# Kernel tuning notes

Hardware: AMD Instinct MI355X
Metric: run time of the kernel (lower is better)

The kernel has to match this reference:

```python
import jax, jax.numpy as jnp
import numpy as np

S, B, E, H = 2048, 4, 512, 8
HD = E // H


def setup_inputs() -> dict:
    key = jax.random.key(0)
    ks = jax.random.split(key, 5)
    scale = 1.0 / np.sqrt(E)
    return {
        "query": jax.random.normal(ks[0], (S, B, E), jnp.float32),
        "key": jax.random.normal(ks[1], (S, B, E), jnp.float32),
        "value": jax.random.normal(ks[2], (S, B, E), jnp.float32),
        "in_proj_weight": jax.random.normal(ks[3], (3 * E, E), jnp.float32) * scale,
        "in_proj_bias": jnp.zeros((3 * E,), jnp.float32),
        "out_proj_weight": jax.random.normal(ks[4], (E, E), jnp.float32) * scale,
        "out_proj_bias": jnp.zeros((E,), jnp.float32),
    }


def reference(query, key, value, in_proj_weight, in_proj_bias, out_proj_weight, out_proj_bias):
    tgt_len, bsz, embed_dim = query.shape
    src_len = key.shape[0]
    # Quirk of this module: first chunk (w_qk) projects BOTH q and k; third chunk projects v.
    w_qk = in_proj_weight[:embed_dim]
    w_v = in_proj_weight[2 * embed_dim:]
    b_qk = in_proj_bias[:embed_dim]
    b_v = in_proj_bias[2 * embed_dim:]
    q = query @ w_qk.T + b_qk          # [S, B, E]
    k = key @ w_qk.T + b_qk
    v = value @ w_v.T + b_v
    # (S, B, E) -> (B*H, S, HD)
    def split_heads(x, n):
        return x.reshape(n, bsz * H, HD).transpose(1, 0, 2)
    q = split_heads(q, tgt_len) / jnp.sqrt(jnp.asarray(HD, q.dtype))
    k = split_heads(k, src_len)
    v = split_heads(v, src_len)
    scores = jnp.einsum("bqd,bkd->bqk", q, k)          # [B*H, S, S] full score matrix
    attn = jax.nn.softmax(scores, axis=-1)
    out = jnp.einsum("bqk,bkd->bqd", attn, v)          # [B*H, S, HD]
    out = out.transpose(1, 0, 2).reshape(tgt_len * bsz, embed_dim)
    out = out @ out_proj_weight.T + out_proj_bias
    return out.reshape(tgt_len, bsz, embed_dim)
```

## Files before the change

### kernel.cpp

```cpp
#include <hip/hip_runtime.h>
#include <hip/hip_bf16.h>

typedef __attribute__((ext_vector_type(8))) short s16x8;
typedef __attribute__((ext_vector_type(4))) short s16x4;
typedef __attribute__((ext_vector_type(4))) float f32x4;

#if __has_builtin(__builtin_amdgcn_exp2f)
#define EXP2F(x) __builtin_amdgcn_exp2f(x)
#else
#define EXP2F(x) exp2f(x)
#endif

#define S_LEN 2048
#define EMB   512
#define MROWS 8192

__device__ __forceinline__ short f2bf(float f) {
    union { float f; unsigned u; } z; z.f = f;
    unsigned r = z.u + 0x7FFF + ((z.u >> 16) & 1);
    return (short)(r >> 16);
}
__device__ __forceinline__ short f2bf_fast(float f) {
    union { float f; unsigned u; } z; z.f = f;
    return (short)((z.u + 0x8000u) >> 16);
}
__device__ __forceinline__ int swzs(int s) { return s ^ ((s >> 3) & 7); }

__device__ __forceinline__ void barrier_fast() {
    asm volatile("s_waitcnt lgkmcnt(0)" ::: "memory");
    __builtin_amdgcn_s_barrier();
    __builtin_amdgcn_sched_barrier(0);
}

__global__ __launch_bounds__(256) void w_to_bf16(const float* __restrict__ W,
                                                 short* __restrict__ wb, int n)
{
    int i = (blockIdx.x * 256 + threadIdx.x) * 8;
    if (i < n) {
        f32x4 a = *(const f32x4*)(W + i);
        f32x4 b = *(const f32x4*)(W + i + 4);
        s16x8 o;
        o[0] = f2bf(a[0]); o[1] = f2bf(a[1]); o[2] = f2bf(a[2]); o[3] = f2bf(a[3]);
        o[4] = f2bf(b[0]); o[5] = f2bf(b[1]); o[6] = f2bf(b[2]); o[7] = f2bf(b[3]);
        *(s16x8*)(wb + i) = o;
    }
}

template<int AF32, int BF32>
__device__ __forceinline__ void gemm_mainloop(const void* __restrict__ Ag,
                                              const void* __restrict__ Bg,
                                              short* sA, short* sB,
                                              f32x4 acc[2][4], int K)
{
    const int tid  = threadIdx.x;
    const int lane = tid & 63;
    const int wv   = tid >> 6;
    const int lsw  = lane ^ ((lane >> 3) & 7);
    const int amt  = (wv >> 1) * 2;
    const int bnt  = (wv & 1) * 4;

    const int brow = tid >> 2, bqd = tid & 3;
    const int boff = swzs((brow >> 4) * 64 + bqd * 16 + (brow & 15)) * 8;
    const int frow = tid >> 3, ffc = tid & 7;
    const int foff = swzs((frow >> 4) * 64 + (ffc >> 1) * 16 + (frow & 15)) * 8
                   + (ffc & 1) * 4;

    f32x4 aF0[2], aF1[2], bF0[2], bF1[2];
    s16x8 aH0, aH1, bH0, bH1;

    auto loadA = [&](int kt, f32x4 fr[2], s16x8& hr) {
        if (AF32) {
            const float* g = (const float*)Ag + (size_t)frow * K + kt + ffc * 4;
            fr[0] = *(const f32x4*)g;
            fr[1] = *(const f32x4*)(g + (size_t)64 * K);
        } else {
            hr = *(const s16x8*)((const short*)Ag + (size_t)brow * K + kt + bqd * 8);
        }
    };
    auto loadB = [&](int kt, f32x4 fr[2], s16x8& hr) {
        if (BF32) {
            const float* g = (const float*)Bg + (size_t)frow * K + kt + ffc * 4;
            fr[0] = *(const f32x4*)g;
            fr[1] = *(const f32x4*)(g + (size_t)64 * K);
        } else {
            hr = *(const s16x8*)((const short*)Bg + (size_t)brow * K + kt + bqd * 8);
        }
    };
    auto commit = [&](short* s, f32x4 fr[2], s16x8& hr, int F32) {
        if (F32) {
#pragma unroll
            for (int p = 0; p < 2; ++p) {
                s16x4 o4;
                o4[0] = f2bf_fast(fr[p][0]); o4[1] = f2bf_fast(fr[p][1]);
                o4[2] = f2bf_fast(fr[p][2]); o4[3] = f2bf_fast(fr[p][3]);
                *(s16x4*)(s + foff + p * 2048) = o4;
            }
        } else {
            *(s16x8*)(s + boff) = hr;
        }
    };
    auto compute = [&](const short* sAc, const short* sBc) {
        s16x8 a[2], b[4];
#pragma unroll
        for (int i = 0; i < 2; ++i)
            a[i] = *(const s16x8*)(sAc + ((amt + i) * 64 + lsw) * 8);
#pragma unroll
        for (int j = 0; j < 4; ++j)
            b[j] = *(const s16x8*)(sBc + ((bnt + j) * 64 + lsw) * 8);
#pragma unroll
        for (int i = 0; i < 2; ++i)
#pragma unroll
            for (int j = 0; j < 4; ++j)
                acc[i][j] = __builtin_amdgcn_mfma_f32_16x16x32_bf16(a[i], b[j], acc[i][j], 0, 0, 0);
    };

    loadA(0, aF0, aH0);  loadB(0, bF0, bH0);
    loadA(32, aF1, aH1); loadB(32, bF1, bH1);
    commit(sA, aF0, aH0, AF32); commit(sB, bF0, bH0, BF32);
    barrier_fast();

    for (int kt = 0; kt < K; kt += 64) {
        const int k2 = (kt + 64 < K) ? kt + 64 : 0;
        loadA(k2, aF0, aH0); loadB(k2, bF0, bH0);
        compute(sA, sB);
        commit(sA + 4096, aF1, aH1, AF32); commit(sB + 4096, bF1, bH1, BF32);
        barrier_fast();
        const int k3 = (kt + 96 < K) ? kt + 96 : 0;
        loadA(k3, aF1, aH1); loadB(k3, bF1, bH1);
        compute(sA + 4096, sB + 4096);
        commit(sA, aF0, aH0, AF32); commit(sB, bF0, bH0, BF32);
        barrier_fast();
    }
}

__global__ __launch_bounds__(512, 4) void qkv_proj(const float* __restrict__ query,
                                                   const float* __restrict__ key,
                                                   const float* __restrict__ value,
                                                   const short* __restrict__ wb,
                                                   const float* __restrict__ bias,
                                                   short* __restrict__ q,
                                                   short* __restrict__ k,
                                                   short* __restrict__ vt)
{
    __shared__ __align__(16) short smem[16384];
    short* sA = smem;
    short* sB = smem + 8192;

    const int z = blockIdx.z;
    const float* X  = (z == 0) ? query : (z == 1) ? key : value;
    const short* Wz = wb   + (z == 2 ? (size_t)1024 * EMB : 0);
    const float* bz = bias + (z == 2 ? 1024 : 0);
    const float scale = (z == 0) ? 0.125f * 1.44269504f : 1.0f;

    const int blockM = blockIdx.x * 128, blockN = blockIdx.y * 128;

    f32x4 acc[2][4];
#pragma unroll
    for (int i = 0; i < 2; ++i)
#pragma unroll
        for (int j = 0; j < 4; ++j)
            acc[i][j] = (f32x4){0.f, 0.f, 0.f, 0.f};

    gemm_mainloop<1, 0>(X + (size_t)blockM * EMB, Wz + (size_t)blockN * EMB,
                        sA, sB, acc, EMB);

    const int tid = threadIdx.x, lane = tid & 63, wv = tid >> 6;
    const int l15 = lane & 15, quad = lane >> 4;
    const int wm = (wv >> 1) * 32, wn = (wv & 1) * 64;

#pragma unroll
    for (int j = 0; j < 4; ++j) {
        int colL = wn + j * 16 + l15;
        float bval = bz[blockN + colL];
        int hL = colL >> 6, hd = colL & 63;
#pragma unroll
        for (int i = 0; i < 2; ++i) {
#pragma unroll
            for (int r = 0; r < 4; ++r) {
                int rowL = wm + i * 16 + quad * 4 + r;
                int b = rowL & 3, sp = rowL >> 2;
                float val = (acc[i][j][r] + bval) * scale;
                int idx;
                if (z == 2) {
                    int R = (b * 2 + hL) * 64 + hd;
                    idx = R * 32 + (((sp >> 3) ^ (R & 3)) << 3) + (sp & 7);
                } else {
                    idx = ((b * 2 + hL) * 32 + sp) * 64 + hd;
                }
                smem[idx] = f2bf(val);
            }
        }
    }
    barrier_fast();

    if (z == 2) {
        int R = tid;
        int b = tid >> 7, hL = (tid >> 6) & 1, hd = tid & 63;
        int h = (blockN >> 6) + hL;
        short* dst = vt + ((size_t)(b * 8 + h) * 64 + hd) * 2048 + (blockM >> 2);
#pragma unroll
        for (int u = 0; u < 4; ++u)
            ((s16x8*)dst)[u] = *(const s16x8*)(smem + R * 32 + ((u ^ (R & 3)) << 3));
    } else {
        const s16x8* src = (const s16x8*)(smem + tid * 32);
        int b = tid >> 7, hL = (tid >> 6) & 1;
        int sp = (tid >> 1) & 31, hdh = (tid & 1) * 32;
        int h = (blockN >> 6) + hL;
        short* dstp = (z == 0) ? q : k;
        short* dst = dstp + ((size_t)(b * 8 + h) * 2048 + (blockM >> 2) + sp) * 64 + hdh;
#pragma unroll
        for (int u = 0; u < 4; ++u) ((s16x8*)dst)[u] = src[u];
    }
}

__global__ __launch_bounds__(256, 2) void flash_attn(const short* __restrict__ q,
                                                     const short* __restrict__ k,
                                                     const short* __restrict__ vt,
                                                     short* __restrict__ attn)
{
    __shared__ __align__(16) short sK[2][8192];
    __shared__ __align__(16) short sV[2][8192];
    const int bh = blockIdx.x;
    const int q0 = blockIdx.y * 128;
    const int tid = threadIdx.x, wv = tid >> 6, lane = tid & 63;
    const int l15 = lane & 15, quad = lane >> 4;
    const int lsw = lane ^ ((lane >> 3) & 7);

    s16x8 qf[2][2];
#pragma unroll
    for (int qr = 0; qr < 2; ++qr) {
        const short* qp = q + ((size_t)(bh * 2048 + q0 + wv * 32 + qr * 16 + l15)) * 64 + quad * 8;
        qf[qr][0] = *(const s16x8*)qp;
        qf[qr][1] = *(const s16x8*)(qp + 32);
    }

    const short* kg = k  + (size_t)bh * 2048 * 64;
    const short* vg = vt + (size_t)bh * 64 * 2048;

    const int rk = tid >> 2, qd = tid & 3;
    const int pr = (rk & 35) | ((rk & 24) >> 1) | ((rk & 4) << 2);
    const int kw0 = swzs((pr >> 4) * 64 + qd * 16 + (pr & 15)) * 8;
    const int vw0 = swzs((rk >> 4) * 64 + qd * 16 + (rk & 15)) * 8;
    const short* kgt = kg + (size_t)rk * 64 + qd * 8;
    const short* vgt = vg + (size_t)rk * 2048 + qd * 8;

    f32x4 o[2][4];
    float ls[2][4];
#pragma unroll
    for (int qr = 0; qr < 2; ++qr)
#pragma unroll
        for (int i = 0; i < 4; ++i) { o[qr][i] = (f32x4){0.f, 0.f, 0.f, 0.f}; ls[qr][i] = 0.f; }

    s16x8 kr[2][2], vr[2][2];
    auto loadT = [&](int kt) {
#pragma unroll
        for (int s = 0; s < 2; ++s) {
            kr[s][0] = *(const s16x8*)(kgt + (size_t)(kt + s * 64) * 64);
            kr[s][1] = *(const s16x8*)(kgt + (size_t)(kt + s * 64) * 64 + 32);
            vr[s][0] = *(const s16x8*)(vgt + kt + s * 64);
            vr[s][1] = *(const s16x8*)(vgt + kt + s * 64 + 32);
        }
    };
    auto commitT = [&](int buf) {
#pragma unroll
        for (int s = 0; s < 2; ++s) {
            *(s16x8*)(sK[buf] + s * 4096 + kw0)        = kr[s][0];
            *(s16x8*)(sK[buf] + s * 4096 + kw0 + 2048) = kr[s][1];
            *(s16x8*)(sV[buf] + s * 4096 + vw0)        = vr[s][0];
            *(s16x8*)(sV[buf] + s * 4096 + vw0 + 2048) = vr[s][1];
        }
    };
    auto computeQK = [&](const short* Kc, f32x4 sc[2][4]) {
#pragma unroll
        for (int ct = 0; ct < 4; ++ct) {
            s16x8 kf0 = *(const s16x8*)(Kc + (ct * 64 + lsw) * 8);
            s16x8 kf1 = *(const s16x8*)(Kc + (ct * 64 + lsw) * 8 + 2048);
#pragma unroll
            for (int qr = 0; qr < 2; ++qr) {
                f32x4 c = (f32x4){0.f, 0.f, 0.f, 0.f};
                c = __builtin_amdgcn_mfma_f32_16x16x32_bf16(kf0, qf[qr][0], c, 0, 0, 0);
                c = __builtin_amdgcn_mfma_f32_16x16x32_bf16(kf1, qf[qr][1], c, 0, 0, 0);
                sc[qr][ct] = c;
            }
        }
    };
    auto softmaxPV = [&](f32x4 sc[2][4], const short* Vc) {
        s16x8 pf[2][2];
#pragma unroll
        for (int qr = 0; qr < 2; ++qr)
#pragma unroll
            for (int c = 0; c < 2; ++c)
#pragma unroll
                for (int h = 0; h < 2; ++h)
#pragma unroll
                    for (int r = 0; r < 4; ++r) {
                        float p = EXP2F(sc[qr][2 * c + h][r]);
                        ls[qr][r] += p;
                        pf[qr][c][h * 4 + r] = f2bf_fast(p);
                    }
#pragma unroll
        for (int nt = 0; nt < 4; ++nt)
#pragma unroll
            for (int c = 0; c < 2; ++c) {
                s16x8 vf = *(const s16x8*)(Vc + ((c * 4 + nt) * 64 + lsw) * 8);
#pragma unroll
                for (int qr = 0; qr < 2; ++qr)
                    o[qr][nt] = __builtin_amdgcn_mfma_f32_16x16x32_bf16(pf[qr][c], vf, o[qr][nt], 0, 0, 0);
            }
    };

    loadT(0);
    commitT(0);
    __syncthreads();

    int cur = 0;
    for (int kt = 0; kt < 2048; kt += 128) {
        loadT((kt + 128) & 2047);

        f32x4 sc0[2][4], sc1[2][4];
        computeQK(sK[cur], sc0);
        computeQK(sK[cur] + 4096, sc1);
        softmaxPV(sc0, sV[cur]);
        softmaxPV(sc1, sV[cur] + 4096);

        commitT(cur ^ 1);
        __syncthreads();
        cur ^= 1;
    }

    const int b = bh >> 3, h = bh & 7;
#pragma unroll
    for (int qr = 0; qr < 2; ++qr) {
        float s = ls[qr][0] + ls[qr][1] + ls[qr][2] + ls[qr][3];
        s += __shfl_xor(s, 16, 64);
        s += __shfl_xor(s, 32, 64);
        float sinv = 1.0f / s;
        float inv[4];
#pragma unroll
        for (int r = 0; r < 4; ++r)
            inv[r] = __shfl(sinv, quad * 20 + r, 64);
#pragma unroll
        for (int r = 0; r < 4; ++r) {
            int srow = q0 + wv * 32 + qr * 16 + quad * 4 + r;
#pragma unroll
            for (int nt = 0; nt < 4; ++nt)
                attn[(size_t)(srow * 4 + b) * 512 + h * 64 + nt * 16 + l15] = f2bf(o[qr][nt][r] * inv[r]);
        }
    }
}

__global__ __launch_bounds__(512, 4) void out_proj(const short* __restrict__ attn,
                                                   const float* __restrict__ W,
                                                   const float* __restrict__ bias,
                                                   float* __restrict__ out)
{
    __shared__ __align__(16) short sA[2 * 4096], sB[2 * 4096];
    const int blockM = blockIdx.x * 128, blockN = blockIdx.y * 128;

    f32x4 acc[2][4];
#pragma unroll
    for (int i = 0; i < 2; ++i)
#pragma unroll
        for (int j = 0; j < 4; ++j)
            acc[i][j] = (f32x4){0.f, 0.f, 0.f, 0.f};

    gemm_mainloop<0, 1>(attn + (size_t)blockM * EMB, W + (size_t)blockN * EMB,
                        sA, sB, acc, EMB);

    const int tid = threadIdx.x, lane = tid & 63, wv = tid >> 6;
    const int l15 = lane & 15, quad = lane >> 4;
    const int wm = (wv >> 1) * 32, wn = (wv & 1) * 64;

#pragma unroll
    for (int j = 0; j < 4; ++j) {
        int col = blockN + wn + j * 16 + l15;
        float bval = bias[col];
#pragma unroll
        for (int i = 0; i < 2; ++i) {
#pragma unroll
            for (int r = 0; r < 4; ++r) {
                int row = blockM + wm + i * 16 + quad * 4 + r;
                out[(size_t)row * 512 + col] = acc[i][j][r] + bval;
            }
        }
    }
}

extern "C" void kernel_launch(void* const* d_in, const int* in_sizes, int n_in,
                              void* d_out, int out_size, void* d_ws, size_t ws_size,
                              hipStream_t stream)
{
    const float* query = (const float*)d_in[0];
    const float* key   = (const float*)d_in[1];
    const float* value = (const float*)d_in[2];
    const float* ipw   = (const float*)d_in[3];
    const float* ipb   = (const float*)d_in[4];
    const float* opw   = (const float*)d_in[5];
    const float* opb   = (const float*)d_in[6];
    float* out = (float*)d_out;

    const size_t NELEM = (size_t)MROWS * EMB;
    short* q    = (short*)d_ws;
    short* k    = q + NELEM;
    short* attn = k + NELEM;
    short* vt   = (short*)d_out;
    short* wb   = (short*)d_out + NELEM;

    w_to_bf16 <<<dim3(384),      256, 0, stream>>>(ipw, wb, 1536 * EMB);
    qkv_proj  <<<dim3(64, 4, 3), 512, 0, stream>>>(query, key, value, wb, ipb, q, k, vt);
    flash_attn<<<dim3(32, 16),   256, 0, stream>>>(q, k, vt, attn);
    out_proj  <<<dim3(64, 4),    512, 0, stream>>>(attn, opw, opb, out);
}
```

Baseline: 181.3 us.

## Fuse all stages into one cooperative persistent kernel with grid syncs

Replaces the four separate launches (weight conversion, QKV projection, flash attention, output projection) with a single cooperative kernel of 256 blocks of 512 threads. Stages are separated by grid.sync. Each block loops over the three QKV projections, and attention now processes 256 query rows per block with 8 waves sharing each K/V tile. The aim is to remove inter-kernel launch gaps and tail effects, and to share K/V tile loads across more query rows. The cost is grid-wide barriers, a fixed grid size that limits parallelism per stage, and higher register and LDS pressure from one kernel covering every phase.

```diff
diff --git a/kernel.cpp b/kernel.cpp
--- a/kernel.cpp
+++ b/kernel.cpp
@@ -1,5 +1,8 @@
 #include <hip/hip_runtime.h>
 #include <hip/hip_bf16.h>
+#include <hip/hip_cooperative_groups.h>
+
+namespace cg = cooperative_groups;
 
 typedef __attribute__((ext_vector_type(8))) short s16x8;
 typedef __attribute__((ext_vector_type(4))) short s16x4;
@@ -11,7 +14,6 @@
 #define EXP2F(x) exp2f(x)
 #endif
 
-#define S_LEN 2048
 #define EMB   512
 #define MROWS 8192
 
@@ -30,20 +32,6 @@
     asm volatile("s_waitcnt lgkmcnt(0)" ::: "memory");
     __builtin_amdgcn_s_barrier();
     __builtin_amdgcn_sched_barrier(0);
-}
-
-__global__ __launch_bounds__(256) void w_to_bf16(const float* __restrict__ W,
-                                                 short* __restrict__ wb, int n)
-{
-    int i = (blockIdx.x * 256 + threadIdx.x) * 8;
-    if (i < n) {
-        f32x4 a = *(const f32x4*)(W + i);
-        f32x4 b = *(const f32x4*)(W + i + 4);
-        s16x8 o;
-        o[0] = f2bf(a[0]); o[1] = f2bf(a[1]); o[2] = f2bf(a[2]); o[3] = f2bf(a[3]);
-        o[4] = f2bf(b[0]); o[5] = f2bf(b[1]); o[6] = f2bf(b[2]); o[7] = f2bf(b[3]);
-        *(s16x8*)(wb + i) = o;
-    }
 }
 
 template<int AF32, int BF32>
@@ -133,26 +121,23 @@
     }
 }
 
-__global__ __launch_bounds__(512, 4) void qkv_proj(const float* __restrict__ query,
-                                                   const float* __restrict__ key,
-                                                   const float* __restrict__ value,
-                                                   const short* __restrict__ wb,
-                                                   const float* __restrict__ bias,
-                                                   short* __restrict__ q,
-                                                   short* __restrict__ k,
-                                                   short* __restrict__ vt)
+__device__ __forceinline__ void qkv_tile(int z, int blockM, int blockN,
+                                         const float* __restrict__ query,
+                                         const float* __restrict__ key,
+                                         const float* __restrict__ value,
+                                         const short* __restrict__ wb,
+                                         const float* __restrict__ ipb,
+                                         short* __restrict__ q,
+                                         short* __restrict__ k,
+                                         short* __restrict__ vt,
+                                         short* smem)
 {
-    __shared__ __align__(16) short smem[16384];
     short* sA = smem;
     short* sB = smem + 8192;
-
-    const int z = blockIdx.z;
     const float* X  = (z == 0) ? query : (z == 1) ? key : value;
-    const short* Wz = wb   + (z == 2 ? (size_t)1024 * EMB : 0);
-    const float* bz = bias + (z == 2 ? 1024 : 0);
+    const short* Wz = wb  + (z == 2 ? (size_t)1024 * EMB : 0);
+    const float* bz = ipb + (z == 2 ? 1024 : 0);
     const float scale = (z == 0) ? 0.125f * 1.44269504f : 1.0f;
-
-    const int blockM = blockIdx.x * 128, blockN = blockIdx.y * 128;
 
     f32x4 acc[2][4];
 #pragma unroll
@@ -213,149 +198,15 @@
     }
 }
 
-__global__ __launch_bounds__(256, 2) void flash_attn(const short* __restrict__ q,
-                                                     const short* __restrict__ k,
-                                                     const short* __restrict__ vt,
-                                                     short* __restrict__ attn)
+__device__ __forceinline__ void out_tile(int blockM, int blockN,
+                                         const short* __restrict__ attn,
+                                         const float* __restrict__ W,
+                                         const float* __restrict__ bias,
+                                         float* __restrict__ out,
+                                         short* smem)
 {
-    __shared__ __align__(16) short sK[2][8192];
-    __shared__ __align__(16) short sV[2][8192];
-    const int bh = blockIdx.x;
-    const int q0 = blockIdx.y * 128;
-    const int tid = threadIdx.x, wv = tid >> 6, lane = tid & 63;
-    const int l15 = lane & 15, quad = lane >> 4;
-    const int lsw = lane ^ ((lane >> 3) & 7);
-
-    s16x8 qf[2][2];
-#pragma unroll
-    for (int qr = 0; qr < 2; ++qr) {
-        const short* qp = q + ((size_t)(bh * 2048 + q0 + wv * 32 + qr * 16 + l15)) * 64 + quad * 8;
-        qf[qr][0] = *(const s16x8*)qp;
-        qf[qr][1] = *(const s16x8*)(qp + 32);
-    }
-
-    const short* kg = k  + (size_t)bh * 2048 * 64;
-    const short* vg = vt + (size_t)bh * 64 * 2048;
-
-    const int rk = tid >> 2, qd = tid & 3;
-    const int pr = (rk & 35) | ((rk & 24) >> 1) | ((rk & 4) << 2);
-    const int kw0 = swzs((pr >> 4) * 64 + qd * 16 + (pr & 15)) * 8;
-    const int vw0 = swzs((rk >> 4) * 64 + qd * 16 + (rk & 15)) * 8;
-    const short* kgt = kg + (size_t)rk * 64 + qd * 8;
-    const short* vgt = vg + (size_t)rk * 2048 + qd * 8;
-
-    f32x4 o[2][4];
-    float ls[2][4];
-#pragma unroll
-    for (int qr = 0; qr < 2; ++qr)
-#pragma unroll
-        for (int i = 0; i < 4; ++i) { o[qr][i] = (f32x4){0.f, 0.f, 0.f, 0.f}; ls[qr][i] = 0.f; }
-
-    s16x8 kr[2][2], vr[2][2];
-    auto loadT = [&](int kt) {
-#pragma unroll
-        for (int s = 0; s < 2; ++s) {
-            kr[s][0] = *(const s16x8*)(kgt + (size_t)(kt + s * 64) * 64);
-            kr[s][1] = *(const s16x8*)(kgt + (size_t)(kt + s * 64) * 64 + 32);
-            vr[s][0] = *(const s16x8*)(vgt + kt + s * 64);
-            vr[s][1] = *(const s16x8*)(vgt + kt + s * 64 + 32);
-        }
-    };
-    auto commitT = [&](int buf) {
-#pragma unroll
-        for (int s = 0; s < 2; ++s) {
-            *(s16x8*)(sK[buf] + s * 4096 + kw0)        = kr[s][0];
-            *(s16x8*)(sK[buf] + s * 4096 + kw0 + 2048) = kr[s][1];
-            *(s16x8*)(sV[buf] + s * 4096 + vw0)        = vr[s][0];
-            *(s16x8*)(sV[buf] + s * 4096 + vw0 + 2048) = vr[s][1];
-        }
-    };
-    auto computeQK = [&](const short* Kc, f32x4 sc[2][4]) {
-#pragma unroll
-        for (int ct = 0; ct < 4; ++ct) {
-            s16x8 kf0 = *(const s16x8*)(Kc + (ct * 64 + lsw) * 8);
-            s16x8 kf1 = *(const s16x8*)(Kc + (ct * 64 + lsw) * 8 + 2048);
-#pragma unroll
-            for (int qr = 0; qr < 2; ++qr) {
-                f32x4 c = (f32x4){0.f, 0.f, 0.f, 0.f};
-                c = __builtin_amdgcn_mfma_f32_16x16x32_bf16(kf0, qf[qr][0], c, 0, 0, 0);
-                c = __builtin_amdgcn_mfma_f32_16x16x32_bf16(kf1, qf[qr][1], c, 0, 0, 0);
-                sc[qr][ct] = c;
-            }
-        }
-    };
-    auto softmaxPV = [&](f32x4 sc[2][4], const short* Vc) {
-        s16x8 pf[2][2];
-#pragma unroll
-        for (int qr = 0; qr < 2; ++qr)
-#pragma unroll
-            for (int c = 0; c < 2; ++c)
-#pragma unroll
-                for (int h = 0; h < 2; ++h)
-#pragma unroll
-                    for (int r = 0; r < 4; ++r) {
-                        float p = EXP2F(sc[qr][2 * c + h][r]);
-                        ls[qr][r] += p;
-                        pf[qr][c][h * 4 + r] = f2bf_fast(p);
-                    }
-#pragma unroll
-        for (int nt = 0; nt < 4; ++nt)
-#pragma unroll
-            for (int c = 0; c < 2; ++c) {
-                s16x8 vf = *(const s16x8*)(Vc + ((c * 4 + nt) * 64 + lsw) * 8);
-#pragma unroll
-                for (int qr = 0; qr < 2; ++qr)
-                    o[qr][nt] = __builtin_amdgcn_mfma_f32_16x16x32_bf16(pf[qr][c], vf, o[qr][nt], 0, 0, 0);
-            }
-    };
-
-    loadT(0);
-    commitT(0);
-    __syncthreads();
-
-    int cur = 0;
-    for (int kt = 0; kt < 2048; kt += 128) {
-        loadT((kt + 128) & 2047);
-
-        f32x4 sc0[2][4], sc1[2][4];
-        computeQK(sK[cur], sc0);
-        computeQK(sK[cur] + 4096, sc1);
-        softmaxPV(sc0, sV[cur]);
-        softmaxPV(sc1, sV[cur] + 4096);
-
-        commitT(cur ^ 1);
-        __syncthreads();
-        cur ^= 1;
-    }
-
-    const int b = bh >> 3, h = bh & 7;
-#pragma unroll
-    for (int qr = 0; qr < 2; ++qr) {
-        float s = ls[qr][0] + ls[qr][1] + ls[qr][2] + ls[qr][3];
-        s += __shfl_xor(s, 16, 64);
-        s += __shfl_xor(s, 32, 64);
-        float sinv = 1.0f / s;
-        float inv[4];
-#pragma unroll
-        for (int r = 0; r < 4; ++r)
-            inv[r] = __shfl(sinv, quad * 20 + r, 64);
-#pragma unroll
-        for (int r = 0; r < 4; ++r) {
-            int srow = q0 + wv * 32 + qr * 16 + quad * 4 + r;
-#pragma unroll
-            for (int nt = 0; nt < 4; ++nt)
-                attn[(size_t)(srow * 4 + b) * 512 + h * 64 + nt * 16 + l15] = f2bf(o[qr][nt][r] * inv[r]);
-        }
-    }
-}
-
-__global__ __launch_bounds__(512, 4) void out_proj(const short* __restrict__ attn,
-                                                   const float* __restrict__ W,
-                                                   const float* __restrict__ bias,
-                                                   float* __restrict__ out)
-{
-    __shared__ __align__(16) short sA[2 * 4096], sB[2 * 4096];
-    const int blockM = blockIdx.x * 128, blockN = blockIdx.y * 128;
+    short* sA = smem;
+    short* sB = smem + 8192;
 
     f32x4 acc[2][4];
 #pragma unroll
@@ -384,6 +235,178 @@
             }
         }
     }
+}
+
+__global__ __launch_bounds__(512, 2) void mega(const float* __restrict__ query,
+                                               const float* __restrict__ key,
+                                               const float* __restrict__ value,
+                                               const float* __restrict__ ipw,
+                                               const float* __restrict__ ipb,
+                                               const float* __restrict__ opw,
+                                               const float* __restrict__ opb,
+                                               float* __restrict__ out,
+                                               short* __restrict__ q,
+                                               short* __restrict__ kk,
+                                               short* __restrict__ attn,
+                                               short* __restrict__ vt,
+                                               short* __restrict__ wb)
+{
+    __shared__ __align__(16) short smem[32768];
+    const int blk = blockIdx.x, tid = threadIdx.x;
+    cg::grid_group grid = cg::this_grid();
+
+    {
+        int i = (blk * 512 + tid) * 8;
+        if (i < 1536 * EMB) {
+            f32x4 a = *(const f32x4*)(ipw + i);
+            f32x4 b = *(const f32x4*)(ipw + i + 4);
+            s16x8 o;
+            o[0] = f2bf(a[0]); o[1] = f2bf(a[1]); o[2] = f2bf(a[2]); o[3] = f2bf(a[3]);
+            o[4] = f2bf(b[0]); o[5] = f2bf(b[1]); o[6] = f2bf(b[2]); o[7] = f2bf(b[3]);
+            *(s16x8*)(wb + i) = o;
+        }
+    }
+    grid.sync();
+
+    {
+        const int x = blk & 63, y = (blk >> 6) & 3;
+        for (int z = 0; z < 3; ++z) {
+            qkv_tile(z, x * 128, y * 128, query, key, value, wb, ipb, q, kk, vt, smem);
+            __syncthreads();
+        }
+    }
+    grid.sync();
+
+    {
+        const int bh  = blk & 31;
+        const int q0b = (blk >> 5) * 256;
+        const int wv  = tid >> 6, lane = tid & 63;
+        const int l15 = lane & 15, quad = lane >> 4;
+        const int lsw = lane ^ ((lane >> 3) & 7);
+
+        short* sKb = smem;
+        short* sVb = smem + 16384;
+
+        s16x8 qf[2][2];
+#pragma unroll
+        for (int qr = 0; qr < 2; ++qr) {
+            const short* qp = q + ((size_t)(bh * 2048 + q0b + wv * 32 + qr * 16 + l15)) * 64 + quad * 8;
+            qf[qr][0] = *(const s16x8*)qp;
+            qf[qr][1] = *(const s16x8*)(qp + 32);
+        }
+
+        const short* kg = kk + (size_t)bh * 2048 * 64;
+        const short* vg = vt + (size_t)bh * 64 * 2048;
+
+        const int rl = tid >> 3, hq = tid & 7;
+        const int prK   = (rl & 35) | ((rl & 24) >> 1) | ((rl & 4) << 2);
+        const int kslot = swzs((prK >> 4) * 64 + (hq & 3) * 16 + (prK & 15)) * 8
+                        + (hq >> 2) * 2048;
+        const short* kgt = kg + (size_t)rl * 64 + hq * 8;
+        const int vslot = swzs(((hq >> 2) * 4 + (rl >> 4)) * 64 + (hq & 3) * 16 + (rl & 15)) * 8;
+        const short* vgt = vg + (size_t)rl * 2048 + hq * 8;
+
+        f32x4 o[2][4];
+        float ls[2][4];
+#pragma unroll
+        for (int qr = 0; qr < 2; ++qr)
+#pragma unroll
+            for (int i = 0; i < 4; ++i) { o[qr][i] = (f32x4){0.f, 0.f, 0.f, 0.f}; ls[qr][i] = 0.f; }
+
+        s16x8 kA, kB, vA, vB;
+        auto loadT = [&](int kt) {
+            kA = *(const s16x8*)(kgt + (size_t)kt * 64);
+            kB = *(const s16x8*)(kgt + (size_t)(kt + 64) * 64);
+            vA = *(const s16x8*)(vgt + kt);
+            vB = *(const s16x8*)(vgt + kt + 64);
+        };
+        auto commitT = [&](int buf) {
+            short* Kb = sKb + buf * 8192;
+            short* Vb = sVb + buf * 8192;
+            *(s16x8*)(Kb + kslot)        = kA;
+            *(s16x8*)(Kb + 4096 + kslot) = kB;
+            *(s16x8*)(Vb + vslot)        = vA;
+            *(s16x8*)(Vb + 4096 + vslot) = vB;
+        };
+        auto computeQK = [&](const short* Kc, f32x4 sc[2][4]) {
+#pragma unroll
+            for (int ct = 0; ct < 4; ++ct) {
+                s16x8 kf0 = *(const s16x8*)(Kc + (ct * 64 + lsw) * 8);
+                s16x8 kf1 = *(const s16x8*)(Kc + (ct * 64 + lsw) * 8 + 2048);
+#pragma unroll
+                for (int qr = 0; qr < 2; ++qr) {
+                    f32x4 c = (f32x4){0.f, 0.f, 0.f, 0.f};
+                    c = __builtin_amdgcn_mfma_f32_16x16x32_bf16(kf0, qf[qr][0], c, 0, 0, 0);
+                    c = __builtin_amdgcn_mfma_f32_16x16x32_bf16(kf1, qf[qr][1], c, 0, 0, 0);
+                    sc[qr][ct] = c;
+                }
+            }
+        };
+        auto softmaxPV = [&](f32x4 sc[2][4], const short* Vc) {
+            s16x8 pf[2][2];
+#pragma unroll
+            for (int qr = 0; qr < 2; ++qr)
+#pragma unroll
+                for (int c = 0; c < 2; ++c)
+#pragma unroll
+                    for (int h = 0; h < 2; ++h)
+#pragma unroll
+                        for (int r = 0; r < 4; ++r) {
+                            float p = EXP2F(sc[qr][2 * c + h][r]);
+                            ls[qr][r] += p;
+                            pf[qr][c][h * 4 + r] = f2bf_fast(p);
+                        }
+#pragma unroll
+            for (int nt = 0; nt < 4; ++nt)
+#pragma unroll
+                for (int c = 0; c < 2; ++c) {
+                    s16x8 vf = *(const s16x8*)(Vc + ((c * 4 + nt) * 64 + lsw) * 8);
+#pragma unroll
+                    for (int qr = 0; qr < 2; ++qr)
+                        o[qr][nt] = __builtin_amdgcn_mfma_f32_16x16x32_bf16(pf[qr][c], vf, o[qr][nt], 0, 0, 0);
+                }
+        };
+
+        loadT(0);
+        commitT(0);
+        __syncthreads();
+
+        int cur = 0;
+        for (int kt = 0; kt < 2048; kt += 128) {
+            loadT((kt + 128) & 2047);
+            f32x4 sc0[2][4], sc1[2][4];
+            computeQK(sKb + cur * 8192, sc0);
+            computeQK(sKb + cur * 8192 + 4096, sc1);
+            softmaxPV(sc0, sVb + cur * 8192);
+            softmaxPV(sc1, sVb + cur * 8192 + 4096);
+            commitT(cur ^ 1);
+            __syncthreads();
+            cur ^= 1;
+        }
+
+        const int b = bh >> 3, h = bh & 7;
+#pragma unroll
+        for (int qr = 0; qr < 2; ++qr) {
+            float s = ls[qr][0] + ls[qr][1] + ls[qr][2] + ls[qr][3];
+            s += __shfl_xor(s, 16, 64);
+            s += __shfl_xor(s, 32, 64);
+            float sinv = 1.0f / s;
+            float inv[4];
+#pragma unroll
+            for (int r = 0; r < 4; ++r)
+                inv[r] = __shfl(sinv, quad * 20 + r, 64);
+#pragma unroll
+            for (int r = 0; r < 4; ++r) {
+                int srow = q0b + wv * 32 + qr * 16 + quad * 4 + r;
+#pragma unroll
+                for (int nt = 0; nt < 4; ++nt)
+                    attn[(size_t)(srow * 4 + b) * 512 + h * 64 + nt * 16 + l15] = f2bf(o[qr][nt][r] * inv[r]);
+            }
+        }
+    }
+    grid.sync();
+
+    out_tile((blk & 63) * 128, (blk >> 6) * 128, attn, opw, opb, out, smem);
 }
 
 extern "C" void kernel_launch(void* const* d_in, const int* in_sizes, int n_in,
@@ -401,13 +424,14 @@
 
     const size_t NELEM = (size_t)MROWS * EMB;
     short* q    = (short*)d_ws;
-    short* k    = q + NELEM;
-    short* attn = k + NELEM;
+    short* kk   = q + NELEM;
+    short* attn = kk + NELEM;
     short* vt   = (short*)d_out;
     short* wb   = (short*)d_out + NELEM;
 
-    w_to_bf16 <<<dim3(384),      256, 0, stream>>>(ipw, wb, 1536 * EMB);
-    qkv_proj  <<<dim3(64, 4, 3), 512, 0, stream>>>(query, key, value, wb, ipb, q, k, vt);
-    flash_attn<<<dim3(32, 16),   256, 0, stream>>>(q, k, vt, attn);
-    out_proj  <<<dim3(64, 4),    512, 0, stream>>>(attn, opw, opb, out);
-}
+    void* args[] = {(void*)&query, (void*)&key, (void*)&value, (void*)&ipw,
+                    (void*)&ipb, (void*)&opw, (void*)&opb, (void*)&out,
+                    (void*)&q, (void*)&kk, (void*)&attn, (void*)&vt, (void*)&wb};
+    hipLaunchCooperativeKernel(reinterpret_cast<void*>(mega), dim3(256), dim3(512),
+                               args, 0, stream);
+}
```

Measured after the change: 296.1 us. 63.3% more time.

## Double GEMM K-step to 128 with wider loads; use hardware bf16 convert in softmax

Applied to the files above, without the earlier changes.

The shared GEMM mainloop now stages 128-wide K tiles instead of 64. Each thread loads 8 contiguous floats (or two 8-element bf16 vectors) per row pair, and LDS doubles to 64KB per block for the projection kernels. The goal is to halve the number of barriers and iterations and to issue wider global loads, at the cost of more registers and LDS, which may lower occupancy under launch_bounds(512,4). Separately, the attention softmax now packs P to bf16 with the library __float2bfloat16 conversion instead of the add-and-shift rounding trick, which may map to a hardware convert instruction.

```diff
diff --git a/kernel.cpp b/kernel.cpp
--- a/kernel.cpp
+++ b/kernel.cpp
@@ -11,7 +11,6 @@
 #define EXP2F(x) exp2f(x)
 #endif
 
-#define S_LEN 2048
 #define EMB   512
 #define MROWS 8192
 
@@ -23,6 +22,11 @@
 __device__ __forceinline__ short f2bf_fast(float f) {
     union { float f; unsigned u; } z; z.f = f;
     return (short)((z.u + 0x8000u) >> 16);
+}
+__device__ __forceinline__ short f2bf_cvt(float f) {
+    union { __hip_bfloat16 h; short s; } cv;
+    cv.h = __float2bfloat16(f);
+    return cv.s;
 }
 __device__ __forceinline__ int swzs(int s) { return s ^ ((s >> 3) & 7); }
 
@@ -59,76 +63,79 @@
     const int amt  = (wv >> 1) * 2;
     const int bnt  = (wv & 1) * 4;
 
-    const int brow = tid >> 2, bqd = tid & 3;
-    const int boff = swzs((brow >> 4) * 64 + bqd * 16 + (brow & 15)) * 8;
-    const int frow = tid >> 3, ffc = tid & 7;
-    const int foff = swzs((frow >> 4) * 64 + (ffc >> 1) * 16 + (frow & 15)) * 8
-                   + (ffc & 1) * 4;
-
-    f32x4 aF0[2], aF1[2], bF0[2], bF1[2];
-    s16x8 aH0, aH1, bH0, bH1;
-
-    auto loadA = [&](int kt, f32x4 fr[2], s16x8& hr) {
-        if (AF32) {
-            const float* g = (const float*)Ag + (size_t)frow * K + kt + ffc * 4;
+    const int srow = tid >> 3, qd = tid & 7;
+    const int offL = (qd >> 2) * 4096
+                   + swzs((srow >> 4) * 64 + (qd & 3) * 16 + (srow & 15)) * 8;
+    const int offH = (qd >> 2) * 4096
+                   + swzs(((srow >> 4) + 4) * 64 + (qd & 3) * 16 + (srow & 15)) * 8;
+
+    f32x4 aF0[4], aF1[4], bF0[4], bF1[4];
+    s16x8 aH0[2], aH1[2], bH0[2], bH1[2];
+
+    auto loadX = [&](const void* G, int kt, f32x4 fr[4], s16x8 hr[2], int F32) {
+        if (F32) {
+            const float* g = (const float*)G + (size_t)srow * K + kt + qd * 8;
             fr[0] = *(const f32x4*)g;
-            fr[1] = *(const f32x4*)(g + (size_t)64 * K);
+            fr[1] = *(const f32x4*)(g + 4);
+            fr[2] = *(const f32x4*)(g + (size_t)64 * K);
+            fr[3] = *(const f32x4*)(g + (size_t)64 * K + 4);
         } else {
-            hr = *(const s16x8*)((const short*)Ag + (size_t)brow * K + kt + bqd * 8);
-        }
-    };
-    auto loadB = [&](int kt, f32x4 fr[2], s16x8& hr) {
-        if (BF32) {
-            const float* g = (const float*)Bg + (size_t)frow * K + kt + ffc * 4;
-            fr[0] = *(const f32x4*)g;
-            fr[1] = *(const f32x4*)(g + (size_t)64 * K);
+            const short* g = (const short*)G + (size_t)srow * K + kt + qd * 8;
+            hr[0] = *(const s16x8*)g;
+            hr[1] = *(const s16x8*)(g + (size_t)64 * K);
+        }
+    };
+    auto commitX = [&](short* s, f32x4 fr[4], s16x8 hr[2], int F32) {
+        if (F32) {
+            s16x8 o;
+            o[0] = f2bf_fast(fr[0][0]); o[1] = f2bf_fast(fr[0][1]);
+            o[2] = f2bf_fast(fr[0][2]); o[3] = f2bf_fast(fr[0][3]);
+            o[4] = f2bf_fast(fr[1][0]); o[5] = f2bf_fast(fr[1][1]);
+            o[6] = f2bf_fast(fr[1][2]); o[7] = f2bf_fast(fr[1][3]);
+            *(s16x8*)(s + offL) = o;
+            o[0] = f2bf_fast(fr[2][0]); o[1] = f2bf_fast(fr[2][1]);
+            o[2] = f2bf_fast(fr[2][2]); o[3] = f2bf_fast(fr[2][3]);
+            o[4] = f2bf_fast(fr[3][0]); o[5] = f2bf_fast(fr[3][1]);
+            o[6] = f2bf_fast(fr[3][2]); o[7] = f2bf_fast(fr[3][3]);
+            *(s16x8*)(s + offH) = o;
         } else {
-            hr = *(const s16x8*)((const short*)Bg + (size_t)brow * K + kt + bqd * 8);
-        }
-    };
-    auto commit = [&](short* s, f32x4 fr[2], s16x8& hr, int F32) {
-        if (F32) {
-#pragma unroll
-            for (int p = 0; p < 2; ++p) {
-                s16x4 o4;
-                o4[0] = f2bf_fast(fr[p][0]); o4[1] = f2bf_fast(fr[p][1]);
-                o4[2] = f2bf_fast(fr[p][2]); o4[3] = f2bf_fast(fr[p][3]);
-                *(s16x4*)(s + foff + p * 2048) = o4;
-            }
-        } else {
-            *(s16x8*)(s + boff) = hr;
+            *(s16x8*)(s + offL) = hr[0];
+            *(s16x8*)(s + offH) = hr[1];
         }
     };
     auto compute = [&](const short* sAc, const short* sBc) {
-        s16x8 a[2], b[4];
-#pragma unroll
-        for (int i = 0; i < 2; ++i)
-            a[i] = *(const s16x8*)(sAc + ((amt + i) * 64 + lsw) * 8);
-#pragma unroll
-        for (int j = 0; j < 4; ++j)
-            b[j] = *(const s16x8*)(sBc + ((bnt + j) * 64 + lsw) * 8);
-#pragma unroll
-        for (int i = 0; i < 2; ++i)
+#pragma unroll
+        for (int h = 0; h < 2; ++h) {
+            s16x8 a[2], b[4];
+#pragma unroll
+            for (int i = 0; i < 2; ++i)
+                a[i] = *(const s16x8*)(sAc + h * 4096 + ((amt + i) * 64 + lsw) * 8);
 #pragma unroll
             for (int j = 0; j < 4; ++j)
-                acc[i][j] = __builtin_amdgcn_mfma_f32_16x16x32_bf16(a[i], b[j], acc[i][j], 0, 0, 0);
-    };
-
-    loadA(0, aF0, aH0);  loadB(0, bF0, bH0);
-    loadA(32, aF1, aH1); loadB(32, bF1, bH1);
-    commit(sA, aF0, aH0, AF32); commit(sB, bF0, bH0, BF32);
+                b[j] = *(const s16x8*)(sBc + h * 4096 + ((bnt + j) * 64 + lsw) * 8);
+#pragma unroll
+            for (int i = 0; i < 2; ++i)
+#pragma unroll
+                for (int j = 0; j < 4; ++j)
+                    acc[i][j] = __builtin_amdgcn_mfma_f32_16x16x32_bf16(a[i], b[j], acc[i][j], 0, 0, 0);
+        }
+    };
+
+    loadX(Ag, 0, aF0, aH0, AF32);  loadX(Bg, 0, bF0, bH0, BF32);
+    loadX(Ag, 64, aF1, aH1, AF32); loadX(Bg, 64, bF1, bH1, BF32);
+    commitX(sA, aF0, aH0, AF32); commitX(sB, bF0, bH0, BF32);
     barrier_fast();
 
-    for (int kt = 0; kt < K; kt += 64) {
-        const int k2 = (kt + 64 < K) ? kt + 64 : 0;
-        loadA(k2, aF0, aH0); loadB(k2, bF0, bH0);
+    for (int kt = 0; kt < K; kt += 128) {
+        const int k2 = (kt + 128 < K) ? kt + 128 : 0;
+        loadX(Ag, k2, aF0, aH0, AF32); loadX(Bg, k2, bF0, bH0, BF32);
         compute(sA, sB);
-        commit(sA + 4096, aF1, aH1, AF32); commit(sB + 4096, bF1, bH1, BF32);
+        commitX(sA + 8192, aF1, aH1, AF32); commitX(sB + 8192, bF1, bH1, BF32);
         barrier_fast();
-        const int k3 = (kt + 96 < K) ? kt + 96 : 0;
-        loadA(k3, aF1, aH1); loadB(k3, bF1, bH1);
-        compute(sA + 4096, sB + 4096);
-        commit(sA, aF0, aH0, AF32); commit(sB, bF0, bH0, BF32);
+        const int k3 = (kt + 192 < K) ? kt + 192 : 0;
+        loadX(Ag, k3, aF1, aH1, AF32); loadX(Bg, k3, bF1, bH1, BF32);
+        compute(sA + 8192, sB + 8192);
+        commitX(sA, aF0, aH0, AF32); commitX(sB, bF0, bH0, BF32);
         barrier_fast();
     }
 }
@@ -142,9 +149,9 @@
                                                    short* __restrict__ k,
                                                    short* __restrict__ vt)
 {
-    __shared__ __align__(16) short smem[16384];
+    __shared__ __align__(16) short smem[32768];
     short* sA = smem;
-    short* sB = smem + 8192;
+    short* sB = smem + 16384;
 
     const int z = blockIdx.z;
     const float* X  = (z == 0) ? query : (z == 1) ? key : value;
@@ -296,7 +303,7 @@
                     for (int r = 0; r < 4; ++r) {
                         float p = EXP2F(sc[qr][2 * c + h][r]);
                         ls[qr][r] += p;
-                        pf[qr][c][h * 4 + r] = f2bf_fast(p);
+                        pf[qr][c][h * 4 + r] = f2bf_cvt(p);
                     }
 #pragma unroll
         for (int nt = 0; nt < 4; ++nt)
@@ -354,7 +361,9 @@
                                                    const float* __restrict__ bias,
                                                    float* __restrict__ out)
 {
-    __shared__ __align__(16) short sA[2 * 4096], sB[2 * 4096];
+    __shared__ __align__(16) short smem[32768];
+    short* sA = smem;
+    short* sB = smem + 16384;
     const int blockM = blockIdx.x * 128, blockN = blockIdx.y * 128;
 
     f32x4 acc[2][4];
```

Measured after the change: 174.9 us. -3.5%, faster.
